# Kernel tuning notes

Measured on AMD Instinct MI355X. Metric: run time of the kernel, lower is better.

## Reference

```python
import jax, jax.numpy as jnp
import numpy as np
import math

# Model dims (see shape_source)
N_EMBD = 2048
QK_H = 128      # per-head qk dim
V_H = 128       # per-head v dim
Q_DIM = N_EMBD                 # 2048 -> 16 query heads
N_HEAD = Q_DIM // QK_H         # 16
KV_HEAD = N_HEAD // 4          # 4 (GQA)
K_DIM = KV_HEAD * QK_H         # 512
V_DIM = KV_HEAD * V_H          # 512
D_KV = K_DIM + V_DIM           # 1024, S6 channel dim
D_STATE = 16                   # S6 state size
DT_RANK = math.ceil(D_KV / 16) # 'auto' -> 64
WINDOW = 512
B, T = 1, 4096


def setup_inputs() -> dict:
    key = jax.random.key(0)
    ks = jax.random.split(key, 8)
    x = jax.random.normal(ks[0], (B, T, N_EMBD), jnp.float32)
    W_attn = jax.random.normal(ks[1], (Q_DIM + K_DIM + V_DIM, N_EMBD), jnp.float32) * 0.02
    # S6 params (canonical Mamba S6 init: A = -exp(A_log), A_log = log(1..N))
    A_log = jnp.log(jnp.arange(1, D_STATE + 1, dtype=jnp.float32))[None, :] * jnp.ones((D_KV, 1), jnp.float32)
    x_proj_w = jax.random.normal(ks[2], (DT_RANK + 2 * D_STATE, D_KV), jnp.float32) * 0.02
    dt_proj_w = jax.random.normal(ks[3], (D_KV, DT_RANK), jnp.float32) * 0.02
    dt_proj_b = jax.random.normal(ks[4], (D_KV,), jnp.float32) * 0.1
    D_param = jnp.ones((D_KV,), jnp.float32)
    W_o = jax.random.normal(ks[5], (N_EMBD, Q_DIM), jnp.float32) * 0.02
    return dict(x=x, W_attn=W_attn, A_log=A_log, x_proj_w=x_proj_w,
                dt_proj_w=dt_proj_w, dt_proj_b=dt_proj_b, D_param=D_param,
                W_o=W_o, window_size=WINDOW)


def s6_scan(u, A_log, x_proj_w, dt_proj_w, dt_proj_b, D_param):
    """Canonical S6 selective scan. u: (B, T, D) -> (B, T, D)."""
    Bb, Tt, D = u.shape
    N = A_log.shape[1]
    dt_rank = dt_proj_w.shape[1]
    x_dbl = jnp.einsum('btd,ed->bte', u, x_proj_w)          # (B,T,dt_rank+2N)
    dt, Bm, Cm = jnp.split(x_dbl, [dt_rank, dt_rank + N], axis=-1)
    delta = jax.nn.softplus(jnp.einsum('btr,dr->btd', dt, dt_proj_w) + dt_proj_b)  # (B,T,D)
    A = -jnp.exp(A_log)                                      # (D,N), negative
    dA = jnp.exp(delta[..., None] * A)                       # (B,T,D,N)
    dBu = delta[..., None] * Bm[:, :, None, :] * u[..., None]  # (B,T,D,N)

    def step(h, inp):
        dA_t, dBu_t, C_t = inp
        h = dA_t * h + dBu_t                                 # (B,D,N)
        y = jnp.einsum('bdn,bn->bd', h, C_t)
        return h, y

    h0 = jnp.zeros((Bb, D, N), u.dtype)
    _, ys = jax.lax.scan(step, h0,
                         (dA.transpose(1, 0, 2, 3), dBu.transpose(1, 0, 2, 3), Cm.transpose(1, 0, 2)))
    y = ys.transpose(1, 0, 2)                                # (B,T,D)
    return y + D_param * u


def sliding_window_attn(q, k, v, window, scale):
    """Causal sliding-window attention; query i attends to j in [i-(window-1), i].
    q: (B,T,H,dh), k/v: (B,T,Hk,dh). Blockwise with one look-back block."""
    Bb, Tt, H, dh = q.shape
    Hk = k.shape[2]
    G = H // Hk
    k = jnp.repeat(k, G, axis=2)
    v = jnp.repeat(v, G, axis=2)
    W = window
    nb = Tt // W
    # (B,H,nb,W,dh)
    qb = q.reshape(Bb, nb, W, H, dh).transpose(0, 3, 1, 2, 4)
    kb = k.reshape(Bb, nb, W, H, dh).transpose(0, 3, 1, 2, 4)
    vb = v.reshape(Bb, nb, W, H, dh).transpose(0, 3, 1, 2, 4)
    # previous block (zeros for first block)
    kprev = jnp.pad(kb, ((0, 0), (0, 0), (1, 0), (0, 0), (0, 0)))[:, :, :nb]
    vprev = jnp.pad(vb, ((0, 0), (0, 0), (1, 0), (0, 0), (0, 0)))[:, :, :nb]
    k2 = jnp.concatenate([kprev, kb], axis=3)                # (B,H,nb,2W,dh)
    v2 = jnp.concatenate([vprev, vb], axis=3)
    scores = jnp.einsum('bhwid,bhwjd->bhwij', qb * scale, k2)  # (B,H,nb,W,2W)
    i = jnp.arange(W)[:, None]
    j = jnp.arange(2 * W)[None, :]
    rel = i + W - j                                          # absolute i - j
    base_mask = (rel >= 0) & (rel <= W - 1)                  # causal & within window
    blk = jnp.arange(nb)[:, None, None]
    valid = base_mask[None] & ((j[None] >= W) | (blk > 0))   # first block: no look-back
    neg = jnp.finfo(jnp.float32).max
    scores = jnp.where(valid[None, None], scores, -neg)
    attn = jax.nn.softmax(scores.astype(jnp.float32), axis=-1).astype(q.dtype)
    out = jnp.einsum('bhwij,bhwjd->bhwid', attn, v2)         # (B,H,nb,W,dh)
    return out.transpose(0, 2, 3, 1, 4).reshape(Bb, Tt, H, dh)


def reference(x, W_attn, A_log, x_proj_w, dt_proj_w, dt_proj_b, D_param, W_o, window_size):
    Bb, Tt, C = x.shape
    qkv = jnp.einsum('btc,oc->bto', x, W_attn)
    q = qkv[..., :Q_DIM]
    kv = qkv[..., Q_DIM:]
    kv = s6_scan(kv, A_log, x_proj_w, dt_proj_w, dt_proj_b, D_param)
    k = kv[..., :K_DIM]
    v = kv[..., K_DIM:]
    q = q.reshape(Bb, Tt, N_HEAD, QK_H)
    k = k.reshape(Bb, Tt, KV_HEAD, QK_H)
    v = v.reshape(Bb, Tt, KV_HEAD, V_H)
    scale = 1.0 / math.sqrt(QK_H)
    y = sliding_window_attn(q, k, v, window_size, scale)     # (B,T,H,v_h)
    y = y.reshape(Bb, Tt, -1)
    return jnp.einsum('bto,no->btn', y, W_o)
```

## Files before the change

### kernel.cpp

```cpp
#include <hip/hip_runtime.h>
#include <hip/hip_bf16.h>

typedef __hip_bfloat16 bf16;
typedef __attribute__((ext_vector_type(8))) short bf16x8;
typedef __attribute__((ext_vector_type(4))) float f32x4;

#define T_SEQ 4096
#define NEMBD 2048
#define QKVD  3072
#define QDIM  2048
#define DKV   1024
#define KDIM  512
#define NH    16
#define DH    128
#define NST   16
#define DTR   64
#define WIN   512
#define NCHUNK 64
#define CLEN   64

__device__ inline float bf2f(bf16 x) { return __bfloat162float(x); }

struct F8 { float v[8]; };

__device__ inline F8 load_b8(const bf16* p) {
  union { uint4 q; unsigned short s[8]; } u;
  u.q = *reinterpret_cast<const uint4*>(p);
  F8 r;
#pragma unroll
  for (int i = 0; i < 8; i++) r.v[i] = __uint_as_float((unsigned)u.s[i] << 16);
  return r;
}

__device__ inline F8 load8(const void* base, size_t idx, int f32flag) {
  if (f32flag) {
    const float4* p = reinterpret_cast<const float4*>((const float*)base + idx);
    float4 a = p[0], b = p[1];
    F8 r;
    r.v[0]=a.x; r.v[1]=a.y; r.v[2]=a.z; r.v[3]=a.w;
    r.v[4]=b.x; r.v[5]=b.y; r.v[6]=b.z; r.v[7]=b.w;
    return r;
  }
  return load_b8((const bf16*)base + idx);
}

__device__ inline float load1(const void* base, size_t idx, int f32flag) {
  return f32flag ? ((const float*)base)[idx] : bf2f(((const bf16*)base)[idx]);
}

__device__ inline unsigned short f2b_bits(float f) {
  bf16 h = __float2bfloat16(f);
  union { bf16 h; unsigned short u; } c; c.h = h; return c.u;
}

__device__ inline ushort4 pack4(float a, float b, float c, float d) {
  ushort4 r; r.x = f2b_bits(a); r.y = f2b_bits(b); r.z = f2b_bits(c); r.w = f2b_bits(d);
  return r;
}

__device__ inline void gld_lds16(const void* g, void* l) {
  __builtin_amdgcn_global_load_lds(
      (const __attribute__((address_space(1))) unsigned int*)g,
      (__attribute__((address_space(3))) unsigned int*)l, 16, 0, 0);
}

__global__ void detect_dtype(const unsigned short* __restrict__ x, int* __restrict__ flag) {
  if (threadIdx.x == 0 && blockIdx.x == 0) {
    int c = 0;
    for (int i = 0; i < 128; i++) {
      float v = __uint_as_float((unsigned)x[i] << 16);
      float a = fabsf(v);
      if (a >= 1e-8f && a <= 1e4f) c++;
    }
    flag[0] = (c >= 120) ? 0 : 1;
  }
}

__global__ __launch_bounds__(256) void cvt_bf16(
    const void* __restrict__ in, const int* __restrict__ dflag,
    unsigned short* __restrict__ out, int n8)
{
  int i = blockIdx.x * 256 + threadIdx.x;
  if (i >= n8) return;
  const int f = dflag[0];
  F8 v = load8(in, (size_t)i * 8, f);
  ushort4* o = (ushort4*)(out + (size_t)i * 8);
  o[0] = pack4(v.v[0], v.v[1], v.v[2], v.v[3]);
  o[1] = pack4(v.v[4], v.v[5], v.v[6], v.v[7]);
}

__global__ __launch_bounds__(256) void gemm_mfma(
    const unsigned short* __restrict__ A, const unsigned short* __restrict__ B,
    int M, int N, int K, int mode,
    bf16* __restrict__ oq, bf16* __restrict__ ou, float* __restrict__ oc)
{
  __shared__ unsigned short As[128 * 32];
  __shared__ unsigned short Bs[128 * 32];
  const int tid = threadIdx.x;
  const int wave = tid >> 6, lane = tid & 63;
  const int quad = lane >> 4, l16 = lane & 15;
  const int bm = blockIdx.y * 128, bn = blockIdx.x * 128;
  const int wm = (wave >> 1) * 64, wn = (wave & 1) * 64;

  const int srow = wave * 32;
  const int lrow = lane >> 2;
  const int lcol = (lane & 3) * 8;

  f32x4 acc[4][4];
#pragma unroll
  for (int i = 0; i < 4; i++)
#pragma unroll
    for (int j = 0; j < 4; j++) acc[i][j] = f32x4{0.f, 0.f, 0.f, 0.f};

  const unsigned short* Ab = A + (size_t)bm * K;
  const unsigned short* Bb = B + (size_t)bn * K;

  for (int k0 = 0; k0 < K; k0 += 32) {
    __syncthreads();
    gld_lds16(Ab + (size_t)(srow + lrow) * K + k0 + lcol,      &As[srow * 32]);
    gld_lds16(Ab + (size_t)(srow + 16 + lrow) * K + k0 + lcol, &As[(srow + 16) * 32]);
    gld_lds16(Bb + (size_t)(srow + lrow) * K + k0 + lcol,      &Bs[srow * 32]);
    gld_lds16(Bb + (size_t)(srow + 16 + lrow) * K + k0 + lcol, &Bs[(srow + 16) * 32]);
    __syncthreads();

    bf16x8 af[4], bfr[4];
#pragma unroll
    for (int i = 0; i < 4; i++)
      af[i] = *(const bf16x8*)&As[(wm + i * 16 + l16) * 32 + quad * 8];
#pragma unroll
    for (int j = 0; j < 4; j++)
      bfr[j] = *(const bf16x8*)&Bs[(wn + j * 16 + l16) * 32 + quad * 8];
#pragma unroll
    for (int i = 0; i < 4; i++)
#pragma unroll
      for (int j = 0; j < 4; j++)
        acc[i][j] = __builtin_amdgcn_mfma_f32_16x16x32_bf16(af[i], bfr[j], acc[i][j], 0, 0, 0);
  }

#pragma unroll
  for (int i = 0; i < 4; i++)
#pragma unroll
    for (int j = 0; j < 4; j++) {
      int gm0 = bm + wm + i * 16 + quad * 4;
      int gn  = bn + wn + j * 16 + l16;
#pragma unroll
      for (int r = 0; r < 4; r++) {
        int gm = gm0 + r;
        float v = acc[i][j][r];
        if (mode == 0) {
          if (gn < QDIM) oq[(size_t)gm * QDIM + gn] = __float2bfloat16(v);
          else           ou[(size_t)gm * DKV + (gn - QDIM)] = __float2bfloat16(v);
        } else {
          oc[(size_t)gm * N + gn] = v;
        }
      }
    }
}

__global__ __launch_bounds__(256) void xdbl_mfma(
    const bf16* __restrict__ u, const unsigned short* __restrict__ xpw_bf,
    float* __restrict__ xd)
{
  __shared__ unsigned short Us[64 * 32];
  __shared__ unsigned short Ws[96 * 32];
  const int tid = threadIdx.x;
  const int wave = tid >> 6, lane = tid & 63;
  const int quad = lane >> 4, l16 = lane & 15;
  const int t0 = blockIdx.x * 64;
  const unsigned short* ub = (const unsigned short*)u;

  f32x4 acc[6];
#pragma unroll
  for (int j = 0; j < 6; j++) acc[j] = f32x4{0.f, 0.f, 0.f, 0.f};

  const int urow = tid >> 2, ucol = (tid & 3) * 8;
  const int wrow0 = tid >> 2, wcol0 = (tid & 3) * 8;
  const int wrow1 = (256 + tid) >> 2;

  uint4 upre = *(const uint4*)(ub + (size_t)(t0 + urow) * DKV + ucol);
  uint4 wpre0 = *(const uint4*)(xpw_bf + (size_t)wrow0 * DKV + wcol0);
  uint4 wpre1 = (tid < 128) ? *(const uint4*)(xpw_bf + (size_t)wrow1 * DKV + wcol0)
                            : uint4{0, 0, 0, 0};

  for (int k0 = 0; k0 < DKV; k0 += 32) {
    __syncthreads();
    *(uint4*)&Us[urow * 32 + ucol] = upre;
    *(uint4*)&Ws[wrow0 * 32 + wcol0] = wpre0;
    if (tid < 128) *(uint4*)&Ws[wrow1 * 32 + wcol0] = wpre1;
    __syncthreads();

    int kn = (k0 + 32 < DKV) ? (k0 + 32) : k0;
    upre  = *(const uint4*)(ub + (size_t)(t0 + urow) * DKV + kn + ucol);
    wpre0 = *(const uint4*)(xpw_bf + (size_t)wrow0 * DKV + kn + wcol0);
    if (tid < 128) wpre1 = *(const uint4*)(xpw_bf + (size_t)wrow1 * DKV + kn + wcol0);

    bf16x8 a = *(const bf16x8*)&Us[(wave * 16 + l16) * 32 + quad * 8];
#pragma unroll
    for (int j = 0; j < 6; j++) {
      bf16x8 b = *(const bf16x8*)&Ws[(j * 16 + l16) * 32 + quad * 8];
      acc[j] = __builtin_amdgcn_mfma_f32_16x16x32_bf16(a, b, acc[j], 0, 0, 0);
    }
  }

#pragma unroll
  for (int j = 0; j < 6; j++)
#pragma unroll
    for (int r = 0; r < 4; r++) {
      int t = t0 + wave * 16 + quad * 4 + r;
      xd[(size_t)t * 96 + j * 16 + l16] = acc[j][r];
    }
}

__global__ __launch_bounds__(256) void delta_mfma(
    const float* __restrict__ xd, const unsigned short* __restrict__ dtw_bf,
    const void* __restrict__ dtb, const int* __restrict__ dflag,
    bf16* __restrict__ delta)
{
  __shared__ unsigned short Xs[64 * 72];
  __shared__ unsigned short Ws[128 * 72];
  const int tid = threadIdx.x;
  const int wave = tid >> 6, lane = tid & 63;
  const int quad = lane >> 4, l16 = lane & 15;
  const int t0 = blockIdx.y * 64, d0 = blockIdx.x * 128;

  for (int e = tid; e < 64 * 8; e += 256) {
    int row = e >> 3, c8 = (e & 7) * 8;
    const float* p = xd + (size_t)(t0 + row) * 96 + c8;
    float4 a = *(const float4*)p, b = *(const float4*)(p + 4);
    *(ushort4*)&Xs[row * 72 + c8]     = pack4(a.x, a.y, a.z, a.w);
    *(ushort4*)&Xs[row * 72 + c8 + 4] = pack4(b.x, b.y, b.z, b.w);
  }
  for (int e = tid; e < 128 * 8; e += 256) {
    int row = e >> 3, c8 = (e & 7) * 8;
    *(uint4*)&Ws[row * 72 + c8] = *(const uint4*)(dtw_bf + (size_t)(d0 + row) * DTR + c8);
  }
  __syncthreads();

  bf16x8 a0 = *(const bf16x8*)&Xs[(wave * 16 + l16) * 72 + quad * 8];
  bf16x8 a1 = *(const bf16x8*)&Xs[(wave * 16 + l16) * 72 + 32 + quad * 8];

  f32x4 acc[8];
#pragma unroll
  for (int j = 0; j < 8; j++) {
    bf16x8 b0 = *(const bf16x8*)&Ws[(j * 16 + l16) * 72 + quad * 8];
    bf16x8 b1 = *(const bf16x8*)&Ws[(j * 16 + l16) * 72 + 32 + quad * 8];
    acc[j] = __builtin_amdgcn_mfma_f32_16x16x32_bf16(a0, b0, f32x4{0.f, 0.f, 0.f, 0.f}, 0, 0, 0);
    acc[j] = __builtin_amdgcn_mfma_f32_16x16x32_bf16(a1, b1, acc[j], 0, 0, 0);
  }

  const int f = dflag[0];
#pragma unroll
  for (int j = 0; j < 8; j++) {
    int d = d0 + j * 16 + l16;
    float bias = load1(dtb, d, f);
#pragma unroll
    for (int r = 0; r < 4; r++) {
      int t = t0 + wave * 16 + quad * 4 + r;
      float v = acc[j][r] + bias;
      float sp = fmaxf(v, 0.f) + log1pf(expf(-fabsf(v)));
      delta[(size_t)t * DKV + d] = __float2bfloat16(sp);
    }
  }
}

__global__ __launch_bounds__(256) void scan_pass1(
    const bf16* __restrict__ delta, const bf16* __restrict__ u,
    const float* __restrict__ xd, const void* __restrict__ A_log,
    const int* __restrict__ dflag, float* __restrict__ Pb, float* __restrict__ Hl)
{
  const int gid = blockIdx.x * 256 + threadIdx.x;
  const int c = gid >> 14;
  const int r = gid & 16383;
  const int d = r >> 4, n = r & 15;
  const int f = dflag[0];
  const float A = -expf(load1(A_log, d * NST + n, f));
  float p = 1.f, h = 0.f;
  const int t0 = c * CLEN;
  for (int tt = 0; tt < CLEN; tt++) {
    int t = t0 + tt;
    float dl = bf2f(delta[(size_t)t * DKV + d]);
    float uu = bf2f(u[(size_t)t * DKV + d]);
    float bm = xd[(size_t)t * 96 + DTR + n];
    float a = expf(dl * A);
    h = a * h + dl * bm * uu;
    p *= a;
  }
  Pb[gid] = p;
  Hl[gid] = h;
}

__global__ __launch_bounds__(256) void scan_combine(
    float* __restrict__ Pb, const float* __restrict__ Hl)
{
  const int idx = blockIdx.x * 256 + threadIdx.x;
  float run = 0.f;
  for (int c = 0; c < NCHUNK; c++) {
    size_t off = (size_t)c * 16384 + idx;
    float p = Pb[off], hl = Hl[off];
    Pb[off] = run;
    run = p * run + hl;
  }
}

__global__ __launch_bounds__(256) void scan_pass2(
    const bf16* __restrict__ delta, bf16* __restrict__ u,
    const float* __restrict__ xd, const void* __restrict__ A_log,
    const void* __restrict__ Dp, const int* __restrict__ dflag,
    const float* __restrict__ Hin)
{
  const int gid = blockIdx.x * 256 + threadIdx.x;
  const int c = gid >> 14;
  const int r = gid & 16383;
  const int d = r >> 4, n = r & 15;
  const int f = dflag[0];
  const float A = -expf(load1(A_log, d * NST + n, f));
  const float dpar = load1(Dp, d, f);
  float h = Hin[gid];
  const int t0 = c * CLEN;
  for (int tt = 0; tt < CLEN; tt++) {
    int t = t0 + tt;
    float dl = bf2f(delta[(size_t)t * DKV + d]);
    float uu = bf2f(u[(size_t)t * DKV + d]);
    float bm = xd[(size_t)t * 96 + DTR + n];
    float cm = xd[(size_t)t * 96 + DTR + NST + n];
    float a = expf(dl * A);
    h = a * h + dl * bm * uu;
    float part = h * cm;
    part += __shfl_xor(part, 1);
    part += __shfl_xor(part, 2);
    part += __shfl_xor(part, 4);
    part += __shfl_xor(part, 8);
    if (n == 0) u[(size_t)t * DKV + d] = __float2bfloat16(part + dpar * uu);
  }
}

__global__ __launch_bounds__(256) void vtrans(
    const bf16* __restrict__ kv, unsigned short* __restrict__ vt)
{
  __shared__ float tile[64][68];
  const int tt0 = blockIdx.x * 64, d0 = blockIdx.y * 64;
  const int tid = threadIdx.x;
  for (int e = tid; e < 64 * 8; e += 256) {
    int row = e >> 3, c8 = (e & 7) * 8;
    F8 v = load_b8(kv + (size_t)(tt0 + row) * DKV + KDIM + d0 + c8);
#pragma unroll
    for (int j = 0; j < 8; j++) tile[row][c8 + j] = v.v[j];
  }
  __syncthreads();
  for (int e = tid; e < 64 * 8; e += 256) {
    int dd = e >> 3, t8 = (e & 7) * 8;
    float vv[8];
#pragma unroll
    for (int j = 0; j < 8; j++) vv[j] = tile[t8 + j][dd];
    ushort4* o = (ushort4*)(vt + (size_t)(d0 + dd) * T_SEQ + tt0 + t8);
    o[0] = pack4(vv[0], vv[1], vv[2], vv[3]);
    o[1] = pack4(vv[4], vv[5], vv[6], vv[7]);
  }
}

__global__ __launch_bounds__(256, 4) void attn_mfma(
    const bf16* __restrict__ q, const bf16* __restrict__ kv,
    const unsigned short* __restrict__ vt, bf16* __restrict__ y)
{
  __shared__ unsigned short Ks[32 * 136];
  __shared__ unsigned short Vts[128 * 40];
  __shared__ unsigned short Ps[4][16 * 40];
  const int tid = threadIdx.x;
  const int wave = tid >> 6, lane = tid & 63;
  const int quad = lane >> 4, l16 = lane & 15;
  const int qt = blockIdx.x, h = blockIdx.y, kvh = h >> 2;
  const int t0 = qt * 64;
  const float scale = 0.088388347648318447f;

  bf16x8 af[4];
#pragma unroll
  for (int s = 0; s < 4; s++)
    af[s] = *(const bf16x8*)(q + (size_t)(t0 + wave * 16 + l16) * QDIM
                             + h * DH + s * 32 + quad * 8);

  const int krow = tid >> 4, kc8 = (tid & 15) * 8;
  const int vrow = tid >> 2, vc8 = (tid & 3) * 8;
  const bf16* kgp = kv + (size_t)kvh * DH;
  const unsigned short* vgp = vt + (size_t)(kvh * DH) * T_SEQ;

  float m_r[4], l_p[4];
  f32x4 O[8];
#pragma unroll
  for (int r = 0; r < 4; r++) { m_r[r] = -1e30f; l_p[r] = 0.f; }
#pragma unroll
  for (int dt = 0; dt < 8; dt++) O[dt] = f32x4{0.f, 0.f, 0.f, 0.f};

  const int kb_start = (t0 > WIN - 1) ? ((t0 - (WIN - 1)) >> 5) : 0;
  const int kb_end = (t0 + 63) >> 5;

  uint4 kp0, kp1, vp0, vp1;
  {
    const int kb = kb_start;
    kp0 = *(const uint4*)(kgp + (size_t)(kb * 32 + krow) * DKV + kc8);
    kp1 = *(const uint4*)(kgp + (size_t)(kb * 32 + 16 + krow) * DKV + kc8);
    vp0 = *(const uint4*)(vgp + (size_t)vrow * T_SEQ + kb * 32 + vc8);
    vp1 = *(const uint4*)(vgp + (size_t)(vrow + 64) * T_SEQ + kb * 32 + vc8);
  }

  for (int kb = kb_start; kb <= kb_end; kb++) {
    __syncthreads();
    *(uint4*)&Ks[krow * 136 + kc8]        = kp0;
    *(uint4*)&Ks[(krow + 16) * 136 + kc8] = kp1;
    *(uint4*)&Vts[vrow * 40 + vc8]        = vp0;
    *(uint4*)&Vts[(vrow + 64) * 40 + vc8] = vp1;
    __syncthreads();

    if (kb < kb_end) {
      const int kn = kb + 1;
      kp0 = *(const uint4*)(kgp + (size_t)(kn * 32 + krow) * DKV + kc8);
      kp1 = *(const uint4*)(kgp + (size_t)(kn * 32 + 16 + krow) * DKV + kc8);
      vp0 = *(const uint4*)(vgp + (size_t)vrow * T_SEQ + kn * 32 + vc8);
      vp1 = *(const uint4*)(vgp + (size_t)(vrow + 64) * T_SEQ + kn * 32 + vc8);
    }

    f32x4 S0 = f32x4{0.f, 0.f, 0.f, 0.f}, S1 = f32x4{0.f, 0.f, 0.f, 0.f};
#pragma unroll
    for (int s = 0; s < 4; s++) {
      bf16x8 b0 = *(const bf16x8*)&Ks[(l16) * 136 + s * 32 + quad * 8];
      bf16x8 b1 = *(const bf16x8*)&Ks[(16 + l16) * 136 + s * 32 + quad * 8];
      S0 = __builtin_amdgcn_mfma_f32_16x16x32_bf16(af[s], b0, S0, 0, 0, 0);
      S1 = __builtin_amdgcn_mfma_f32_16x16x32_bf16(af[s], b1, S1, 0, 0, 0);
    }

    const int ka0 = kb * 32 + l16;
    const int ka1 = ka0 + 16;
    const bool full = (kb * 32 >= t0 + 63 - (WIN - 1)) && (kb * 32 + 31 <= t0);

    float v0r[4], v1r[4];
    bool x0r[4], x1r[4];
    bool ok = true;
#pragma unroll
    for (int r = 0; r < 4; r++) {
      int qa = t0 + wave * 16 + quad * 4 + r;
      float v0 = S0[r] * scale, v1 = S1[r] * scale;
      bool x0 = true, x1 = true;
      if (!full) {
        x0 = (ka0 <= qa) && (ka0 > qa - WIN);
        x1 = (ka1 <= qa) && (ka1 > qa - WIN);
        if (!x0) v0 = -1e30f;
        if (!x1) v1 = -1e30f;
      }
      v0r[r] = v0; v1r[r] = v1; x0r[r] = x0; x1r[r] = x1;
      ok = ok && (fmaxf(v0, v1) <= m_r[r] + 8.f);
    }

    if (!__all((int)ok)) {
#pragma unroll
      for (int r = 0; r < 4; r++) {
        float rm = fmaxf(v0r[r], v1r[r]);
        rm = fmaxf(rm, __shfl_xor(rm, 1));
        rm = fmaxf(rm, __shfl_xor(rm, 2));
        rm = fmaxf(rm, __shfl_xor(rm, 4));
        rm = fmaxf(rm, __shfl_xor(rm, 8));
        float mnew = fmaxf(m_r[r], rm);
        float al = __expf(m_r[r] - mnew);
        m_r[r] = mnew;
        l_p[r] *= al;
#pragma unroll
        for (int dt = 0; dt < 8; dt++) O[dt][r] *= al;
      }
    }

#pragma unroll
    for (int r = 0; r < 4; r++) {
      float p0 = x0r[r] ? __expf(v0r[r] - m_r[r]) : 0.f;
      float p1 = x1r[r] ? __expf(v1r[r] - m_r[r]) : 0.f;
      l_p[r] += p0 + p1;
      Ps[wave][(quad * 4 + r) * 40 + l16]      = f2b_bits(p0);
      Ps[wave][(quad * 4 + r) * 40 + 16 + l16] = f2b_bits(p1);
    }

    bf16x8 pa = *(const bf16x8*)&Ps[wave][l16 * 40 + quad * 8];
#pragma unroll
    for (int dt = 0; dt < 8; dt++) {
      bf16x8 b = *(const bf16x8*)&Vts[(dt * 16 + l16) * 40 + quad * 8];
      O[dt] = __builtin_amdgcn_mfma_f32_16x16x32_bf16(pa, b, O[dt], 0, 0, 0);
    }
  }

  float inv[4];
#pragma unroll
  for (int r = 0; r < 4; r++) {
    float l = l_p[r];
    l += __shfl_xor(l, 1);
    l += __shfl_xor(l, 2);
    l += __shfl_xor(l, 4);
    l += __shfl_xor(l, 8);
    inv[r] = 1.f / l;
  }
#pragma unroll
  for (int dt = 0; dt < 8; dt++)
#pragma unroll
    for (int r = 0; r < 4; r++) {
      int row = t0 + wave * 16 + quad * 4 + r;
      y[(size_t)row * QDIM + h * DH + dt * 16 + l16] = __float2bfloat16(O[dt][r] * inv[r]);
    }
}

extern "C" void kernel_launch(void* const* d_in, const int* in_sizes, int n_in,
                              void* d_out, int out_size, void* d_ws, size_t ws_size,
                              hipStream_t stream)
{
  const void* x      = d_in[0];
  const void* W_attn = d_in[1];
  const void* A_log  = d_in[2];
  const void* xpw    = d_in[3];
  const void* dtw    = d_in[4];
  const void* dtb    = d_in[5];
  const void* Dp     = d_in[6];
  const void* W_o    = d_in[7];

  char* ws = (char*)d_ws;
  int*   dflag = (int*)ws;   ws += 256;
  bf16*  u     = (bf16*)ws;  ws += (size_t)T_SEQ * DKV * 2;
  float* xd    = (float*)ws; ws += (size_t)T_SEQ * 96 * 4;
  char*  yreg  = ws;
  bf16*  delta = (bf16*)ws;  ws += (size_t)T_SEQ * DKV * 2;
  float* Pb    = (float*)ws; ws += (size_t)NCHUNK * DKV * NST * 4;
  float* Hl    = (float*)ws; ws += (size_t)NCHUNK * DKV * NST * 4;
  unsigned short* x_bf  = (unsigned short*)ws; ws += (size_t)T_SEQ * NEMBD * 2;
  unsigned short* wa_bf = (unsigned short*)ws; ws += (size_t)QKVD * NEMBD * 2;
  unsigned short* wo_bf = (unsigned short*)ws; ws += (size_t)NEMBD * QDIM * 2;
  unsigned short* vt    = (unsigned short*)ws; ws += (size_t)KDIM * T_SEQ * 2;
  unsigned short* xpw_bf = (unsigned short*)ws; ws += (size_t)96 * DKV * 2;
  unsigned short* dtw_bf = (unsigned short*)ws; ws += (size_t)DKV * DTR * 2;
  bf16*  y     = (bf16*)yreg;

  bf16*  q_bf = (bf16*)d_out;
  float* out  = (float*)d_out;

  detect_dtype<<<1, 64, 0, stream>>>((const unsigned short*)x, dflag);
  cvt_bf16<<<(T_SEQ * NEMBD / 8 + 255) / 256, 256, 0, stream>>>(x, dflag, x_bf, T_SEQ * NEMBD / 8);
  cvt_bf16<<<(QKVD * NEMBD / 8 + 255) / 256, 256, 0, stream>>>(W_attn, dflag, wa_bf, QKVD * NEMBD / 8);
  cvt_bf16<<<(NEMBD * QDIM / 8 + 255) / 256, 256, 0, stream>>>(W_o, dflag, wo_bf, NEMBD * QDIM / 8);
  cvt_bf16<<<(96 * DKV / 8 + 255) / 256, 256, 0, stream>>>(xpw, dflag, xpw_bf, 96 * DKV / 8);
  cvt_bf16<<<(DKV * DTR / 8 + 255) / 256, 256, 0, stream>>>(dtw, dflag, dtw_bf, DKV * DTR / 8);

  gemm_mfma<<<dim3(QKVD / 128, T_SEQ / 128), 256, 0, stream>>>(
      x_bf, wa_bf, T_SEQ, QKVD, NEMBD, 0, q_bf, u, nullptr);
  xdbl_mfma<<<T_SEQ / 64, 256, 0, stream>>>(u, xpw_bf, xd);
  delta_mfma<<<dim3(DKV / 128, T_SEQ / 64), 256, 0, stream>>>(xd, dtw_bf, dtb, dflag, delta);
  scan_pass1<<<4096, 256, 0, stream>>>(delta, u, xd, A_log, dflag, Pb, Hl);
  scan_combine<<<64, 256, 0, stream>>>(Pb, Hl);
  scan_pass2<<<4096, 256, 0, stream>>>(delta, u, xd, A_log, Dp, dflag, Pb);
  vtrans<<<dim3(T_SEQ / 64, KDIM / 64), 256, 0, stream>>>(u, vt);
  attn_mfma<<<dim3(T_SEQ / 64, NH), 256, 0, stream>>>(q_bf, u, vt, y);
  gemm_mfma<<<dim3(QDIM / 128, T_SEQ / 128), 256, 0, stream>>>(
      (const unsigned short*)y, wo_bf, T_SEQ, QDIM, QDIM, 1, nullptr, nullptr, out);
}
```

Measured before the change: 456.9 us.

## Replace GEMM with 128x256 double-buffered, swizzled, interleaved-prefetch MFMA kernel

Replaces the 128x128 single-buffered GEMM, which used a K-step of 32 and two full barriers per step, with a 512-thread 128x256 tile kernel. It uses a K-step of 64, two LDS buffers, and XOR-swizzled LDS layout to avoid bank conflicts. Global-to-LDS loads for future tiles are interleaved between four MFMA phases, with s_setprio raised around the MFMA bursts, so memory traffic overlaps compute. The cost is higher LDS use (96KB per block) and many extra barriers. The hand-tuned vmcnt waits are fragile, and B tiles are loaded two steps ahead into the buffer currently being read.

```diff
diff --git a/kernel.cpp b/kernel.cpp
--- a/kernel.cpp
+++ b/kernel.cpp
@@ -89,22 +89,28 @@
   o[1] = pack4(v.v[4], v.v[5], v.v[6], v.v[7]);
 }
 
-__global__ __launch_bounds__(256) void gemm_mfma(
+__global__ __launch_bounds__(512, 2) void gemm_wide(
     const unsigned short* __restrict__ A, const unsigned short* __restrict__ B,
     int M, int N, int K, int mode,
     bf16* __restrict__ oq, bf16* __restrict__ ou, float* __restrict__ oc)
 {
-  __shared__ unsigned short As[128 * 32];
-  __shared__ unsigned short Bs[128 * 32];
+  __shared__ unsigned short lds[2][384 * 64];
   const int tid = threadIdx.x;
   const int wave = tid >> 6, lane = tid & 63;
   const int quad = lane >> 4, l16 = lane & 15;
-  const int bm = blockIdx.y * 128, bn = blockIdx.x * 128;
-  const int wm = (wave >> 1) * 64, wn = (wave & 1) * 64;
-
-  const int srow = wave * 32;
-  const int lrow = lane >> 2;
-  const int lcol = (lane & 3) * 8;
+  const int wm = wave >> 2, wn = wave & 3;
+  const int bm = blockIdx.y * 128, bn = blockIdx.x * 256;
+
+  const int lrow = lane >> 3;
+  const int lslot = (lane & 7) ^ lrow;
+  const unsigned short* Abase = A + (size_t)(bm + wave * 8 + lrow) * K + lslot * 8;
+  const unsigned short* Bbase = B + (size_t)(bn + wave * 8 + lrow) * K + lslot * 8;
+
+  const int x7 = l16 & 7;
+  const int s0 = ((0 + quad) ^ x7) * 8;
+  const int s1 = ((4 + quad) ^ x7) * 8;
+  const int arow0 = (wm * 64 + l16) * 64;
+  const int brow0 = (128 + wn * 64 + l16) * 64;
 
   f32x4 acc[4][4];
 #pragma unroll
@@ -112,41 +118,101 @@
 #pragma unroll
     for (int j = 0; j < 4; j++) acc[i][j] = f32x4{0.f, 0.f, 0.f, 0.f};
 
-  const unsigned short* Ab = A + (size_t)bm * K;
-  const unsigned short* Bb = B + (size_t)bn * K;
-
-  for (int k0 = 0; k0 < K; k0 += 32) {
-    __syncthreads();
-    gld_lds16(Ab + (size_t)(srow + lrow) * K + k0 + lcol,      &As[srow * 32]);
-    gld_lds16(Ab + (size_t)(srow + 16 + lrow) * K + k0 + lcol, &As[(srow + 16) * 32]);
-    gld_lds16(Bb + (size_t)(srow + lrow) * K + k0 + lcol,      &Bs[srow * 32]);
-    gld_lds16(Bb + (size_t)(srow + 16 + lrow) * K + k0 + lcol, &Bs[(srow + 16) * 32]);
-    __syncthreads();
-
-    bf16x8 af[4], bfr[4];
-#pragma unroll
-    for (int i = 0; i < 4; i++)
-      af[i] = *(const bf16x8*)&As[(wm + i * 16 + l16) * 32 + quad * 8];
-#pragma unroll
-    for (int j = 0; j < 4; j++)
-      bfr[j] = *(const bf16x8*)&Bs[(wn + j * 16 + l16) * 32 + quad * 8];
-#pragma unroll
-    for (int i = 0; i < 4; i++)
-#pragma unroll
-      for (int j = 0; j < 4; j++)
-        acc[i][j] = __builtin_amdgcn_mfma_f32_16x16x32_bf16(af[i], bfr[j], acc[i][j], 0, 0, 0);
-  }
-
-#pragma unroll
-  for (int i = 0; i < 4; i++)
-#pragma unroll
-    for (int j = 0; j < 4; j++) {
-      int gm0 = bm + wm + i * 16 + quad * 4;
-      int gn  = bn + wn + j * 16 + l16;
+  const int NT = K >> 6;
+
+  gld_lds16(Abase,                          &lds[0][(0   + wave * 8) * 64]);
+  gld_lds16(Abase + (size_t)64 * K,         &lds[0][(64  + wave * 8) * 64]);
+  gld_lds16(Bbase,                          &lds[0][(128 + wave * 8) * 64]);
+  gld_lds16(Bbase + (size_t)64 * K,         &lds[0][(192 + wave * 8) * 64]);
+  gld_lds16(Bbase + (size_t)128 * K,        &lds[0][(256 + wave * 8) * 64]);
+  gld_lds16(Bbase + (size_t)192 * K,        &lds[0][(320 + wave * 8) * 64]);
+  gld_lds16(Bbase + 64,                     &lds[1][(128 + wave * 8) * 64]);
+  gld_lds16(Bbase + (size_t)64 * K + 64,    &lds[1][(192 + wave * 8) * 64]);
+  gld_lds16(Bbase + (size_t)128 * K + 64,   &lds[1][(256 + wave * 8) * 64]);
+  gld_lds16(Bbase + (size_t)192 * K + 64,   &lds[1][(320 + wave * 8) * 64]);
+  asm volatile("s_waitcnt vmcnt(4)" ::: "memory");
+  __builtin_amdgcn_sched_barrier(0);
+  __builtin_amdgcn_s_barrier();
+
+#define MM(m, n) \
+  acc[m][n] = __builtin_amdgcn_mfma_f32_16x16x32_bf16(aF[m][0], bF[n][0], acc[m][n], 0, 0, 0); \
+  acc[m][n] = __builtin_amdgcn_mfma_f32_16x16x32_bf16(aF[m][1], bF[n][1], acc[m][n], 0, 0, 0);
+
+  for (int g = 0; g < NT; ++g) {
+    const unsigned short* L = lds[g & 1];
+    unsigned short* Ln = lds[(g & 1) ^ 1];
+    const bool stA = (g + 1) < NT;
+    const bool stB = (g + 2) < NT;
+    const size_t kA = (size_t)(g + 1) * 64;
+    const size_t kB = (size_t)(g + 2) * 64;
+
+    bf16x8 aF[4][2], bF[4][2];
+
+    aF[0][0] = *(const bf16x8*)&L[arow0 +    0 + s0];
+    aF[0][1] = *(const bf16x8*)&L[arow0 +    0 + s1];
+    aF[1][0] = *(const bf16x8*)&L[arow0 + 1024 + s0];
+    aF[1][1] = *(const bf16x8*)&L[arow0 + 1024 + s1];
+    bF[0][0] = *(const bf16x8*)&L[brow0 +    0 + s0];
+    bF[0][1] = *(const bf16x8*)&L[brow0 +    0 + s1];
+    bF[1][0] = *(const bf16x8*)&L[brow0 + 1024 + s0];
+    bF[1][1] = *(const bf16x8*)&L[brow0 + 1024 + s1];
+    if (stA) gld_lds16(Abase + kA, &Ln[(0 + wave * 8) * 64]);
+    __builtin_amdgcn_s_barrier();
+    __builtin_amdgcn_s_setprio(1);
+    MM(0,0); MM(0,1); MM(1,0); MM(1,1);
+    __builtin_amdgcn_s_setprio(0);
+    __builtin_amdgcn_s_barrier();
+
+    bF[2][0] = *(const bf16x8*)&L[brow0 + 2048 + s0];
+    bF[2][1] = *(const bf16x8*)&L[brow0 + 2048 + s1];
+    bF[3][0] = *(const bf16x8*)&L[brow0 + 3072 + s0];
+    bF[3][1] = *(const bf16x8*)&L[brow0 + 3072 + s1];
+    if (stA) gld_lds16(Abase + (size_t)64 * K + kA, &Ln[(64 + wave * 8) * 64]);
+    __builtin_amdgcn_s_barrier();
+    __builtin_amdgcn_s_setprio(1);
+    MM(0,2); MM(0,3); MM(1,2); MM(1,3);
+    __builtin_amdgcn_s_setprio(0);
+    __builtin_amdgcn_s_barrier();
+
+    aF[2][0] = *(const bf16x8*)&L[arow0 + 2048 + s0];
+    aF[2][1] = *(const bf16x8*)&L[arow0 + 2048 + s1];
+    aF[3][0] = *(const bf16x8*)&L[arow0 + 3072 + s0];
+    aF[3][1] = *(const bf16x8*)&L[arow0 + 3072 + s1];
+    if (stB) {
+      gld_lds16(Bbase + kB,                  (unsigned short*)&L[(128 + wave * 8) * 64]);
+      gld_lds16(Bbase + (size_t)64 * K + kB, (unsigned short*)&L[(192 + wave * 8) * 64]);
+    }
+    __builtin_amdgcn_s_barrier();
+    __builtin_amdgcn_s_setprio(1);
+    MM(2,0); MM(2,1); MM(3,0); MM(3,1);
+    __builtin_amdgcn_s_setprio(0);
+    __builtin_amdgcn_s_barrier();
+
+    if (stB) {
+      gld_lds16(Bbase + (size_t)128 * K + kB, (unsigned short*)&L[(256 + wave * 8) * 64]);
+      gld_lds16(Bbase + (size_t)192 * K + kB, (unsigned short*)&L[(320 + wave * 8) * 64]);
+    }
+    __builtin_amdgcn_s_barrier();
+    __builtin_amdgcn_s_setprio(1);
+    MM(2,2); MM(2,3); MM(3,2); MM(3,3);
+    __builtin_amdgcn_s_setprio(0);
+    if (stB) { asm volatile("s_waitcnt vmcnt(4)" ::: "memory"); }
+    else     { asm volatile("s_waitcnt vmcnt(0)" ::: "memory"); }
+    __builtin_amdgcn_sched_barrier(0);
+    __builtin_amdgcn_s_barrier();
+  }
+#undef MM
+
+#pragma unroll
+  for (int m = 0; m < 4; m++)
+#pragma unroll
+    for (int n = 0; n < 4; n++) {
+      int gm0 = bm + wm * 64 + m * 16 + quad * 4;
+      int gn  = bn + wn * 64 + n * 16 + l16;
 #pragma unroll
       for (int r = 0; r < 4; r++) {
         int gm = gm0 + r;
-        float v = acc[i][j][r];
+        float v = acc[m][n][r];
         if (mode == 0) {
           if (gn < QDIM) oq[(size_t)gm * QDIM + gn] = __float2bfloat16(v);
           else           ou[(size_t)gm * DKV + (gn - QDIM)] = __float2bfloat16(v);
@@ -541,7 +607,7 @@
   cvt_bf16<<<(96 * DKV / 8 + 255) / 256, 256, 0, stream>>>(xpw, dflag, xpw_bf, 96 * DKV / 8);
   cvt_bf16<<<(DKV * DTR / 8 + 255) / 256, 256, 0, stream>>>(dtw, dflag, dtw_bf, DKV * DTR / 8);
 
-  gemm_mfma<<<dim3(QKVD / 128, T_SEQ / 128), 256, 0, stream>>>(
+  gemm_wide<<<dim3(QKVD / 256, T_SEQ / 128), 512, 0, stream>>>(
       x_bf, wa_bf, T_SEQ, QKVD, NEMBD, 0, q_bf, u, nullptr);
   xdbl_mfma<<<T_SEQ / 64, 256, 0, stream>>>(u, xpw_bf, xd);
   delta_mfma<<<dim3(DKV / 128, T_SEQ / 64), 256, 0, stream>>>(xd, dtw_bf, dtb, dflag, delta);
@@ -550,6 +616,6 @@
   scan_pass2<<<4096, 256, 0, stream>>>(delta, u, xd, A_log, Dp, dflag, Pb);
   vtrans<<<dim3(T_SEQ / 64, KDIM / 64), 256, 0, stream>>>(u, vt);
   attn_mfma<<<dim3(T_SEQ / 64, NH), 256, 0, stream>>>(q_bf, u, vt, y);
-  gemm_mfma<<<dim3(QDIM / 128, T_SEQ / 128), 256, 0, stream>>>(
+  gemm_wide<<<dim3(QDIM / 256, T_SEQ / 128), 512, 0, stream>>>(
       (const unsigned short*)y, wo_bf, T_SEQ, QDIM, QDIM, 1, nullptr, nullptr, out);
 }
```

Result: faster. 445.7 us (-2.5%).
